# Kernel tuning notes

Measured on AMD Instinct MI355X. Metric: run time of the kernel, lower is better.

The kernel has to match this reference:

```python
import jax, jax.numpy as jnp
import numpy as np

B = 16; L_IN = 512; D_MODEL = 512; N_HEAD = 8; D_K = 128; D_V = 128
D_FF = 2048; N_LAYER = 4; WINDOW = (4, 4, 4); INNER = 5; COV = 4; NUM_SEQ = 128
N_LVL = len(WINDOW) + 1


def _build_mask_sizes():
    # Pyraformer get_mask: intra-scale band + inter-scale parent/child links.
    all_size = [L_IN]
    for w in WINDOW:
        all_size.append(all_size[-1] // w)
    L = sum(all_size)
    vis = np.zeros((L, L), dtype=bool)
    iw = INNER // 2
    starts = [0]
    for s in all_size:
        starts.append(starts[-1] + s)
    for li, sz in enumerate(all_size):
        s = starts[li]
        for i in range(s, s + sz):
            vis[i, max(i - iw, s):min(i + iw + 1, s + sz)] = True
    for li in range(1, len(all_size)):
        s = starts[li]
        for i in range(s, s + all_size[li]):
            l = (s - all_size[li - 1]) + (i - s) * WINDOW[li - 1]
            if i == s + all_size[li] - 1:
                r = s
            else:
                r = (s - all_size[li - 1]) + (i - s + 1) * WINDOW[li - 1]
            vis[i, l:r] = True
            vis[l:r, i] = True
    return ~vis, all_size  # True = blocked


def _build_indexes(all_size):
    # Pyraformer refer_points: for each fine position, its ancestor at each scale.
    idx = np.zeros((L_IN, len(all_size)), dtype=np.int64)
    for i in range(L_IN):
        idx[i, 0] = i
        former = i
        for j in range(1, len(all_size)):
            start = sum(all_size[:j])
            inner = former - (start - all_size[j - 1])
            former = start + min(inner // WINDOW[j - 1], all_size[j] - 1)
            idx[i, j] = former
    return idx


def _layer_norm(x, g, b, eps=1e-5):
    m = x.mean(-1, keepdims=True)
    v = x.var(-1, keepdims=True)
    return (x - m) / jnp.sqrt(v + eps) * g + b


def _conv1d(x, w, stride):  # x: [B,C,L], w: [O,I,K]
    return jax.lax.conv_general_dilated(x, w, (stride,), 'VALID',
                                        dimension_numbers=('NCH', 'OIH', 'NCH'))


def _forward(x, cov_w, cov_b, data_conv_w, down_w, down_b, conv_w, conv_b, bn_g, bn_b,
             up_w, up_b, bln_g, bln_b, wq, wk, wv, fc_w, ln1_g, ln1_b,
             ffn_w1, ffn_b1, ffn_w2, ffn_b2, ln2_g, ln2_b, attn_mask, gather_idx):
    Bsz = x.shape[0]
    # SingleStepEmbedding
    covs = jnp.concatenate([x[:, :, 1:1 + COV], (x[:, :, -1] / NUM_SEQ - 0.5)[..., None]], -1)
    cov_emb = covs @ cov_w + cov_b
    data = x[:, :, 0][:, None, :]                      # [B,1,L]
    data = jnp.concatenate([data[:, :, -1:], data, data[:, :, :1]], -1)  # circular pad k=3
    data_emb = _conv1d(data, data_conv_w, 1).transpose(0, 2, 1)          # [B,L,D]
    i = jnp.arange(D_MODEL)
    vec = jnp.power(10000.0, 2.0 * (i // 2) / D_MODEL)
    ang = jnp.arange(L_IN)[:, None] / vec
    pos_emb = jnp.where(i % 2 == 0, jnp.sin(ang), jnp.cos(ang))
    seq = cov_emb + data_emb + pos_emb[None]
    # Bottleneck_Construct (down -> strided convs -> up -> concat -> LN)
    tmp = (seq @ down_w + down_b).transpose(0, 2, 1)   # [B,d_k,L]
    outs = []
    for s in range(len(WINDOW)):
        tmp = _conv1d(tmp, conv_w[s], WINDOW[s]) + conv_b[s][None, :, None]
        mu = tmp.mean((0, 2), keepdims=True)
        var = tmp.var((0, 2), keepdims=True)
        tmp = (tmp - mu) / jnp.sqrt(var + 1e-5) * bn_g[s][None, :, None] + bn_b[s][None, :, None]
        tmp = jax.nn.elu(tmp)
        outs.append(tmp)
    pyr = jnp.concatenate(outs, axis=2).transpose(0, 2, 1) @ up_w + up_b
    enc = _layer_norm(jnp.concatenate([seq, pyr], axis=1), bln_g, bln_b)  # [B,Ltot,D]
    Lt = enc.shape[1]
    scale = np.float32(1.0 / np.sqrt(D_K))
    for l in range(N_LAYER):
        q = (enc @ wq[l]).reshape(Bsz, Lt, N_HEAD, D_K).transpose(0, 2, 1, 3)
        k = (enc @ wk[l]).reshape(Bsz, Lt, N_HEAD, D_K).transpose(0, 2, 1, 3)
        v = (enc @ wv[l]).reshape(Bsz, Lt, N_HEAD, D_V).transpose(0, 2, 1, 3)
        scores = jnp.einsum('bhqd,bhkd->bhqk', q, k) * scale
        scores = jnp.where(attn_mask[None, None], -1e9, scores)
        attn = jax.nn.softmax(scores, -1)
        o = jnp.einsum('bhqk,bhkd->bhqd', attn, v).transpose(0, 2, 1, 3).reshape(Bsz, Lt, N_HEAD * D_V)
        enc = _layer_norm(o @ fc_w[l] + enc, ln1_g[l], ln1_b[l])  # post-norm
        h = jax.nn.gelu(enc @ ffn_w1[l] + ffn_b1[l], approximate=False) @ ffn_w2[l] + ffn_b2[l]
        enc = _layer_norm(enc + h, ln2_g[l], ln2_b[l])
    # refer_points gather: [B, L_IN, N_LVL*D]
    out = enc[:, gather_idx.reshape(-1), :].reshape(Bsz, L_IN, N_LVL * D_MODEL)
    return out


def setup_inputs() -> dict:
    key = jax.random.key(0)
    ks = iter(jax.random.split(key, 64))

    def nrm(shape, scale=0.02):
        return (jax.random.normal(next(ks), shape) * scale).astype(jnp.float32)

    covs = jax.random.normal(next(ks), (B, L_IN, COV + 1), jnp.float32)
    ids = jax.random.randint(next(ks), (B, L_IN), 0, NUM_SEQ).astype(jnp.float32)
    x = jnp.concatenate([covs, ids[..., None]], -1)  # col0=data, 1..COV=covs, last=series id
    mask_np, all_size = _build_mask_sizes()
    idx = _build_indexes(all_size)
    nw = len(WINDOW)
    return dict(
        x=x,
        cov_w=nrm((COV + 1, D_MODEL)), cov_b=jnp.zeros((D_MODEL,), jnp.float32),
        data_conv_w=nrm((D_MODEL, 1, 3)),
        down_w=nrm((D_MODEL, D_K)), down_b=jnp.zeros((D_K,), jnp.float32),
        conv_w=nrm((nw, D_K, D_K, WINDOW[0])), conv_b=jnp.zeros((nw, D_K), jnp.float32),
        bn_g=jnp.ones((nw, D_K), jnp.float32), bn_b=jnp.zeros((nw, D_K), jnp.float32),
        up_w=nrm((D_K, D_MODEL)), up_b=jnp.zeros((D_MODEL,), jnp.float32),
        bln_g=jnp.ones((D_MODEL,), jnp.float32), bln_b=jnp.zeros((D_MODEL,), jnp.float32),
        wq=nrm((N_LAYER, D_MODEL, N_HEAD * D_K)), wk=nrm((N_LAYER, D_MODEL, N_HEAD * D_K)),
        wv=nrm((N_LAYER, D_MODEL, N_HEAD * D_V)), fc_w=nrm((N_LAYER, N_HEAD * D_V, D_MODEL)),
        ln1_g=jnp.ones((N_LAYER, D_MODEL), jnp.float32), ln1_b=jnp.zeros((N_LAYER, D_MODEL), jnp.float32),
        ffn_w1=nrm((N_LAYER, D_MODEL, D_FF)), ffn_b1=jnp.zeros((N_LAYER, D_FF), jnp.float32),
        ffn_w2=nrm((N_LAYER, D_FF, D_MODEL)), ffn_b2=jnp.zeros((N_LAYER, D_MODEL), jnp.float32),
        ln2_g=jnp.ones((N_LAYER, D_MODEL), jnp.float32), ln2_b=jnp.zeros((N_LAYER, D_MODEL), jnp.float32),
        attn_mask=jnp.asarray(mask_np),
        gather_idx=jnp.asarray(idx),
    )


def reference(x, cov_w, cov_b, data_conv_w, down_w, down_b, conv_w, conv_b, bn_g, bn_b,
              up_w, up_b, bln_g, bln_b, wq, wk, wv, fc_w, ln1_g, ln1_b,
              ffn_w1, ffn_b1, ffn_w2, ffn_b2, ln2_g, ln2_b, attn_mask, gather_idx):
    return _forward(x, cov_w, cov_b, data_conv_w, down_w, down_b, conv_w, conv_b, bn_g, bn_b,
                    up_w, up_b, bln_g, bln_b, wq, wk, wv, fc_w, ln1_g, ln1_b,
                    ffn_w1, ffn_b1, ffn_w2, ffn_b2, ln2_g, ln2_b, attn_mask, gather_idx)
```

## Files before the change

kernel.cpp:

```cpp
#include <hip/hip_runtime.h>
#include <math.h>

typedef unsigned short u16;
typedef unsigned int u32;
typedef __attribute__((ext_vector_type(8))) short s16x8;
typedef __attribute__((ext_vector_type(4))) float f32x4;
typedef __attribute__((ext_vector_type(4))) u32 u32x4;
typedef __attribute__((ext_vector_type(2))) u32 u32x2;

#define LT 680

static __device__ __forceinline__ float bf2f(u16 u) {
  u32 v = ((u32)u) << 16;
  return __builtin_bit_cast(float, v);
}
static __device__ __forceinline__ u16 f2bf(float f) {
  u32 u = __builtin_bit_cast(u32, f);
  u32 r = (u + 0x7FFFu + ((u >> 16) & 1u)) >> 16;
  return (u16)r;
}
static __device__ __forceinline__ float lo16(u32 u) {
  return __builtin_bit_cast(float, u << 16);
}
static __device__ __forceinline__ float hi16(u32 u) {
  return __builtin_bit_cast(float, u & 0xFFFF0000u);
}

static __device__ __forceinline__ void gload16(const u16* g, u16* l) {
  __builtin_amdgcn_global_load_lds(
      (const __attribute__((address_space(1))) u32*)g,
      (__attribute__((address_space(3))) u32*)l, 16, 0, 0);
}

__global__ void detect_k(const u32* __restrict__ blng, int* __restrict__ flag) {
  if (threadIdx.x == 0 && blockIdx.x == 0)
    *flag = (blng[0] == 0x3F803F80u) ? 1 : 0;
}

struct CvtArgs {
  const void* src[20];
  float* dst[20];
  int pre[21];
};

__global__ __launch_bounds__(256) void cvtall_k(CvtArgs a, const int* __restrict__ flag) {
  int i = blockIdx.x * 256 + threadIdx.x;
  if (i >= a.pre[20]) return;
  int s = 0;
#pragma unroll
  for (int k = 1; k <= 20; ++k)
    if (i >= a.pre[k]) s = k;
  int j = i - a.pre[s];
  bool isb = (*flag != 0);
  a.dst[s][j] = isb ? bf2f(((const u16*)a.src[s])[j]) : ((const float*)a.src[s])[j];
}

__global__ __launch_bounds__(256) void tc2_k(const void* __restrict__ S,
                                             u16* __restrict__ D, int K, int N,
                                             size_t sstride, size_t dstride,
                                             const int* __restrict__ flag) {
  __shared__ u16 t[32][33];
  size_t soff = (size_t)blockIdx.z * sstride;
  D += (size_t)blockIdx.z * dstride;
  int nb = blockIdx.x * 32, kb = blockIdx.y * 32;
  int lx = threadIdx.x & 31, ly = threadIdx.x >> 5;
  bool isb = (*flag != 0);
#pragma unroll
  for (int i = 0; i < 4; ++i) {
    size_t idx = soff + (size_t)(kb + ly + 8 * i) * N + nb + lx;
    t[ly + 8 * i][lx] = isb ? ((const u16*)S)[idx] : f2bf(((const float*)S)[idx]);
  }
  __syncthreads();
#pragma unroll
  for (int i = 0; i < 4; ++i)
    D[(size_t)(nb + ly + 8 * i) * K + kb + lx] = t[lx][ly + 8 * i];
}

static __device__ __forceinline__ void reduce2_256(float& a, float& b, float* sm) {
#pragma unroll
  for (int o = 32; o; o >>= 1) { a += __shfl_xor(a, o); b += __shfl_xor(b, o); }
  int w = threadIdx.x >> 6, ln = threadIdx.x & 63;
  if (ln == 0) { sm[w] = a; sm[4 + w] = b; }
  __syncthreads();
  a = sm[0] + sm[1] + sm[2] + sm[3];
  b = sm[4] + sm[5] + sm[6] + sm[7];
  __syncthreads();
}

__global__ __launch_bounds__(256) void emb_k(
    const float* __restrict__ x, const float* __restrict__ covw,
    const float* __restrict__ covb, const float* __restrict__ dw,
    float* __restrict__ seq) {
  int r = blockIdx.x;
  int b = r >> 9, l = r & 511;
  int base = r * 6;
  float c0 = x[base + 1], c1 = x[base + 2];
  float c2 = x[base + 3], c3 = x[base + 4];
  float c4 = x[base + 5] * 0.0078125f - 0.5f;
  int lm = (l + 511) & 511, lp = (l + 1) & 511;
  float dm = x[((b << 9) + lm) * 6];
  float d0 = x[base];
  float dp = x[((b << 9) + lp) * 6];
  for (int d = threadIdx.x; d < 512; d += 256) {
    float cov = c0 * covw[d] + c1 * covw[512 + d] +
                c2 * covw[1024 + d] + c3 * covw[1536 + d] +
                c4 * covw[2048 + d] + covb[d];
    float cv = dm * dw[d * 3] + d0 * dw[d * 3 + 1] + dp * dw[d * 3 + 2];
    float ex = (float)(2 * (d >> 1)) * (1.0f / 512.0f);
    float vec = powf(10000.0f, ex);
    float ang = (float)l / vec;
    float pos = (d & 1) ? cosf(ang) : sinf(ang);
    seq[((size_t)r << 9) + d] = cov + cv + pos;
  }
}

__global__ void tconv_k(const float* __restrict__ w, float* __restrict__ wt) {
  int e = blockIdx.x * 256 + threadIdx.x;
  if (e >= 3 * 512 * 128) return;
  int o = e & 127, ik = (e >> 7) & 511, s = e >> 16;
  wt[e] = w[s * 65536 + o * 512 + ik];
}

__global__ __launch_bounds__(256) void gemm_k(
    const float* __restrict__ A, const float* __restrict__ Bw,
    const float* __restrict__ bias, float* __restrict__ C,
    int M, int N, int K, int act) {
  __shared__ float As[16][64];
  __shared__ float Bs[16][64];
  int tid = threadIdx.x;
  int m0 = blockIdx.y * 64, n0 = blockIdx.x * 64;
  int tx = tid & 15, ty = tid >> 4;
  int la_r = tid >> 2, la_c = (tid & 3) << 2;
  int lb_r = tid >> 4, lb_c = (tid & 15) << 2;
  float acc[4][4] = {};
  for (int k0 = 0; k0 < K; k0 += 16) {
    float4 av = *reinterpret_cast<const float4*>(A + (size_t)(m0 + la_r) * K + k0 + la_c);
    As[la_c + 0][la_r] = av.x;
    As[la_c + 1][la_r] = av.y;
    As[la_c + 2][la_r] = av.z;
    As[la_c + 3][la_r] = av.w;
    float4 bv = *reinterpret_cast<const float4*>(Bw + (size_t)(k0 + lb_r) * N + n0 + lb_c);
    Bs[lb_r][lb_c + 0] = bv.x;
    Bs[lb_r][lb_c + 1] = bv.y;
    Bs[lb_r][lb_c + 2] = bv.z;
    Bs[lb_r][lb_c + 3] = bv.w;
    __syncthreads();
#pragma unroll
    for (int kk = 0; kk < 16; ++kk) {
      float4 a4 = *reinterpret_cast<const float4*>(&As[kk][ty << 2]);
      float4 b4 = *reinterpret_cast<const float4*>(&Bs[kk][tx << 2]);
      float ar[4] = {a4.x, a4.y, a4.z, a4.w};
      float br[4] = {b4.x, b4.y, b4.z, b4.w};
#pragma unroll
      for (int i = 0; i < 4; ++i)
#pragma unroll
        for (int j = 0; j < 4; ++j) acc[i][j] = fmaf(ar[i], br[j], acc[i][j]);
    }
    __syncthreads();
  }
  float bj[4] = {0.f, 0.f, 0.f, 0.f};
  if (bias) {
#pragma unroll
    for (int j = 0; j < 4; ++j) bj[j] = bias[n0 + (tx << 2) + j];
  }
#pragma unroll
  for (int i = 0; i < 4; ++i) {
    float4 o;
    float* op = reinterpret_cast<float*>(&o);
#pragma unroll
    for (int j = 0; j < 4; ++j) op[j] = acc[i][j] + bj[j];
    *reinterpret_cast<float4*>(C + (size_t)(m0 + (ty << 2) + i) * N + n0 + (tx << 2)) = o;
  }
}

static __device__ __forceinline__ f32x4 mfma16(s16x8 a, s16x8 b, f32x4 c) {
  return __builtin_amdgcn_mfma_f32_16x16x32_bf16(a, b, c, 0, 0, 0);
}

__global__ __launch_bounds__(256) void mgemm_k(
    const u16* __restrict__ A, const u16* __restrict__ BT,
    const float* __restrict__ bias, void* __restrict__ C,
    int M, int N, int K, int flags) {
  __shared__ char smem[49152];
  float* st = (float*)smem;
  int tid = threadIdx.x;

  int nN = N >> 7;
  int nwg = gridDim.x;
  int bid = blockIdx.x;
  int qq = nwg >> 3, rr = nwg & 7;
  int xcd = bid & 7, lin = bid >> 3;
  int s_ = (xcd < rr ? xcd * (qq + 1) : rr * (qq + 1) + (xcd - rr) * qq) + lin;
  int m0 = (s_ / nN) << 7, n0 = (s_ % nN) << 7;

  int l = tid & 63, wid = tid >> 6;
  int wr = wid >> 1, wc = wid & 1;
  f32x4 acc[4][4];
#pragma unroll
  for (int i = 0; i < 4; ++i)
#pragma unroll
    for (int j = 0; j < 4; ++j)
#pragma unroll
      for (int r = 0; r < 4; ++r) acc[i][j][r] = 0.f;

  int L8 = l >> 3;
  int p0_ = (l & 7) ^ L8;
  int rloc = 2 * L8 + (p0_ >> 2);
  int cel = (p0_ & 3) << 3;
  const u16* Ag0 = A + (size_t)m0 * K;
  const u16* Bg0 = BT + (size_t)n0 * K;

  auto STAGE = [&](int c, int kt) {
    u16* Ad = (u16*)smem + c * 8192;
    u16* Bd = Ad + 4096;
#pragma unroll
    for (int i = 0; i < 2; ++i) {
      int rg = wid * 32 + i * 16 + rloc;
      gload16(Ag0 + (size_t)rg * K + kt + cel, &Ad[(wid * 16 + i * 8) * 64]);
      gload16(Bg0 + (size_t)rg * K + kt + cel, &Bd[(wid * 16 + i * 8) * 64]);
    }
  };

  int sfrag = (((l & 1) << 2) + (l >> 4)) ^ (((l & 15) >> 1));
  int lhalf = (l & 15) >> 1;

  int nt = K >> 5;
  STAGE(0, 0);
  STAGE(1, 32);
  for (int t = 0; t < nt; ++t) {
    int cur = t % 3;
    if (t + 2 < nt) {
      STAGE((t + 2) % 3, (t + 2) << 5);
      asm volatile("s_waitcnt vmcnt(8)" ::: "memory");
    } else if (t + 1 < nt) {
      asm volatile("s_waitcnt vmcnt(4)" ::: "memory");
    } else {
      asm volatile("s_waitcnt vmcnt(0)" ::: "memory");
    }
    __builtin_amdgcn_s_barrier();
    const u16* Asb = (const u16*)smem + cur * 8192;
    const u16* Bsb = Asb + 4096;
    s16x8 af[4];
#pragma unroll
    for (int fr = 0; fr < 4; ++fr)
      af[fr] = *reinterpret_cast<const s16x8*>(
          &Asb[(wr * 32 + fr * 8 + lhalf) * 64 + sfrag * 8]);
#pragma unroll
    for (int fc = 0; fc < 4; ++fc) {
      s16x8 bf = *reinterpret_cast<const s16x8*>(
          &Bsb[(wc * 32 + fc * 8 + lhalf) * 64 + sfrag * 8]);
#pragma unroll
      for (int fr = 0; fr < 4; ++fr)
        acc[fr][fc] = mfma16(af[fr], bf, acc[fr][fc]);
    }
    asm volatile("s_waitcnt lgkmcnt(0)" ::: "memory");
    __builtin_amdgcn_s_barrier();
  }

  int cl = l & 15, rg2 = l >> 4;
  float bj[4];
#pragma unroll
  for (int fc = 0; fc < 4; ++fc)
    bj[fc] = bias ? bias[n0 + wc * 64 + fc * 16 + cl] : 0.f;
  int sr2 = tid >> 3;
  int scg = (tid & 7) << 4;
  int growb = m0 + ((sr2 >> 4) << 6) + (sr2 & 15);
#pragma unroll
  for (int fr = 0; fr < 4; ++fr) {
#pragma unroll
    for (int fc = 0; fc < 4; ++fc) {
      int col = wc * 64 + fc * 16 + cl;
#pragma unroll
      for (int r = 0; r < 4; ++r) {
        float v = acc[fr][fc][r] + bj[fc];
        if (flags & 2) {
          float zz = 1.5957691f * fmaf(0.044715f * v, v * v, v);
          v = v / (1.0f + __expf(-zz));
        }
        st[(wr * 16 + rg2 * 4 + r) * 132 + col] = v;
      }
    }
    __syncthreads();
    int gr = growb + fr * 16;
    if (flags & 1) {
      u32x4 o0, o1;
      u16* p0 = (u16*)&o0; u16* p1 = (u16*)&o1;
#pragma unroll
      for (int i = 0; i < 8; ++i) p0[i] = f2bf(st[sr2 * 132 + scg + i]);
#pragma unroll
      for (int i = 0; i < 8; ++i) p1[i] = f2bf(st[sr2 * 132 + scg + 8 + i]);
      u16* dst = (u16*)C + (size_t)gr * N + n0 + scg;
      __builtin_nontemporal_store(o0, reinterpret_cast<u32x4*>(dst));
      __builtin_nontemporal_store(o1, reinterpret_cast<u32x4*>(dst + 8));
    } else {
      float* dst = (float*)C + (size_t)gr * N + n0 + scg;
#pragma unroll
      for (int i = 0; i < 4; ++i)
        __builtin_nontemporal_store(
            *reinterpret_cast<const f32x4*>(&st[sr2 * 132 + scg + 4 * i]),
            reinterpret_cast<f32x4*>(dst + 4 * i));
    }
    __syncthreads();
  }
}

__global__ __launch_bounds__(256) void mg64_k(
    const u16* __restrict__ A, const u16* __restrict__ BT,
    const float* __restrict__ bias, float* __restrict__ C,
    int M, int N, int K) {
  __shared__ char smem[49152];
  float* st = (float*)smem;
  int tid = threadIdx.x;

  int nN = N >> 6;
  int nwg = gridDim.x;
  int bid = blockIdx.x;
  int qq = nwg >> 3, rr = nwg & 7;
  int xcd = bid & 7, lin = bid >> 3;
  int s_ = (xcd < rr ? xcd * (qq + 1) : rr * (qq + 1) + (xcd - rr) * qq) + lin;
  int m0 = (s_ / nN) << 6, n0 = (s_ % nN) << 6;

  int l = tid & 63, wid = tid >> 6;
  f32x4 acc[4];
#pragma unroll
  for (int j = 0; j < 4; ++j)
#pragma unroll
    for (int r = 0; r < 4; ++r) acc[j][r] = 0.f;

  int row8 = l >> 3, cp = l & 7;
  int cg = (cp ^ (row8 & 7)) << 3;
  const u16* Ag0 = A + (size_t)m0 * K;
  const u16* Bg0 = BT + (size_t)n0 * K;

  auto STAGE = [&](int c, int kt) {
    u16* Ad = (u16*)smem + c * 8192;
    u16* Bd = Ad + 4096;
#pragma unroll
    for (int i = 0; i < 2; ++i) {
      int r = wid * 16 + i * 8 + row8;
      gload16(Ag0 + (size_t)r * K + kt + cg, &Ad[(wid * 16 + i * 8) * 64]);
      gload16(Bg0 + (size_t)r * K + kt + cg, &Bd[(wid * 16 + i * 8) * 64]);
    }
  };

  int nt = K >> 6;
  STAGE(0, 0);
  STAGE(1, 64);
  for (int t = 0; t < nt; ++t) {
    int cur = t % 3;
    if (t + 2 < nt) {
      STAGE((t + 2) % 3, (t + 2) << 6);
      asm volatile("s_waitcnt vmcnt(8)" ::: "memory");
    } else if (t + 1 < nt) {
      asm volatile("s_waitcnt vmcnt(4)" ::: "memory");
    } else {
      asm volatile("s_waitcnt vmcnt(0)" ::: "memory");
    }
    __builtin_amdgcn_s_barrier();
    const u16* Asb = (const u16*)smem + cur * 8192;
    const u16* Bsb = Asb + 4096;
#pragma unroll
    for (int kk = 0; kk < 2; ++kk) {
      int kc = ((kk * 4 + (l >> 4)) ^ (l & 7)) * 8;
      s16x8 af = *reinterpret_cast<const s16x8*>(
          &Asb[(wid * 16 + (l & 15)) * 64 + kc]);
#pragma unroll
      for (int fc = 0; fc < 4; ++fc) {
        s16x8 bf = *reinterpret_cast<const s16x8*>(
            &Bsb[(fc * 16 + (l & 15)) * 64 + kc]);
        acc[fc] = mfma16(af, bf, acc[fc]);
      }
    }
    asm volatile("s_waitcnt lgkmcnt(0)" ::: "memory");
    __builtin_amdgcn_s_barrier();
  }

  int cl = l & 15, rg = l >> 4;
  float bj[4];
#pragma unroll
  for (int fc = 0; fc < 4; ++fc)
    bj[fc] = bias ? bias[n0 + fc * 16 + cl] : 0.f;
#pragma unroll
  for (int fc = 0; fc < 4; ++fc)
#pragma unroll
    for (int r = 0; r < 4; ++r)
      st[(wid * 16 + rg * 4 + r) * 80 + fc * 16 + cl] = acc[fc][r] + bj[fc];
  __syncthreads();
  int lr = tid >> 2;
  int lq = (tid & 3) << 2;
  float* dst = C + (size_t)(m0 + lr) * N + n0;
#pragma unroll
  for (int i = 0; i < 4; ++i)
    __builtin_nontemporal_store(
        *reinterpret_cast<const f32x4*>(&st[lr * 80 + lq + 16 * i]),
        reinterpret_cast<f32x4*>(dst + lq + 16 * i));
}

__global__ void im2col_k(const float* __restrict__ Y, float* __restrict__ X,
                         int Ti, int To) {
  int e = blockIdx.x * 256 + threadIdx.x;
  int ik = e & 511;
  int bt = e >> 9;
  int b = bt / To, t = bt - b * To;
  int i = ik >> 2, k = ik & 3;
  X[e] = Y[((size_t)(b * Ti + (t << 2) + k) << 7) + i];
}

__global__ __launch_bounds__(256) void bnelu_k(float* __restrict__ Y,
                                               const float* __restrict__ g,
                                               const float* __restrict__ be, int Ms) {
  __shared__ float sm[8];
  int ch = blockIdx.x;
  float s = 0.f, s2 = 0.f;
  for (int i = threadIdx.x; i < Ms; i += 256) {
    float v = Y[((size_t)i << 7) + ch];
    s += v; s2 += v * v;
  }
  reduce2_256(s, s2, sm);
  float mu = s / (float)Ms;
  float var = s2 / (float)Ms - mu * mu;
  float inv = rsqrtf(var + 1e-5f);
  float ga = g[ch], bb = be[ch];
  for (int i = threadIdx.x; i < Ms; i += 256) {
    float v = (Y[((size_t)i << 7) + ch] - mu) * inv * ga + bb;
    Y[((size_t)i << 7) + ch] = (v > 0.f) ? v : (expf(v) - 1.0f);
  }
}

__global__ void scat_k(const float* __restrict__ Y, float* __restrict__ cat,
                       int Ts, int off) {
  int e = blockIdx.x * 256 + threadIdx.x;
  int i = e & 127;
  int bt = e >> 7;
  int b = bt / Ts, t = bt - b * Ts;
  cat[((size_t)(b * 168 + off + t) << 7) + i] = Y[e];
}

__global__ __launch_bounds__(256) void catln_k(
    const float* __restrict__ seq, const float* __restrict__ pyr,
    const float* __restrict__ g, const float* __restrict__ be,
    float* __restrict__ out, u16* __restrict__ outb) {
  __shared__ float sm[8];
  int row = blockIdx.x;
  int b = row / LT, j = row - b * LT;
  const float* src = (j < 512) ? (seq + ((size_t)(b * 512 + j) << 9))
                               : (pyr + ((size_t)(b * 168 + j - 512) << 9));
  int t = threadIdx.x;
  float x0 = src[t], x1 = src[t + 256];
  float s = x0 + x1, s2 = x0 * x0 + x1 * x1;
  reduce2_256(s, s2, sm);
  float mu = s * 0.001953125f;
  float var = s2 * 0.001953125f - mu * mu;
  float inv = rsqrtf(var + 1e-5f);
  size_t ob = (size_t)row << 9;
  float v0 = (x0 - mu) * inv * g[t] + be[t];
  float v1 = (x1 - mu) * inv * g[t + 256] + be[t + 256];
  out[ob + t] = v0; out[ob + t + 256] = v1;
  outb[ob + t] = f2bf(v0); outb[ob + t + 256] = f2bf(v1);
}

__global__ __launch_bounds__(256) void lnres_k(
    const float* __restrict__ A, const float* __restrict__ R,
    const float* __restrict__ g, const float* __restrict__ be,
    float* __restrict__ O, u16* __restrict__ Ob) {
  __shared__ float sm[8];
  int row = blockIdx.x;
  size_t base = (size_t)row << 9;
  int t = threadIdx.x;
  float x0 = A[base + t] + R[base + t];
  float x1 = A[base + t + 256] + R[base + t + 256];
  float s = x0 + x1, s2 = x0 * x0 + x1 * x1;
  reduce2_256(s, s2, sm);
  float mu = s * 0.001953125f;
  float var = s2 * 0.001953125f - mu * mu;
  float inv = rsqrtf(var + 1e-5f);
  float v0 = (x0 - mu) * inv * g[t] + be[t];
  float v1 = (x1 - mu) * inv * g[t + 256] + be[t + 256];
  O[base + t] = v0; O[base + t + 256] = v1;
  Ob[base + t] = f2bf(v0); Ob[base + t + 256] = f2bf(v1);
}

__global__ __launch_bounds__(256) void attn_k(const u16* __restrict__ QKV,
                                              u16* __restrict__ O) {
  int cpx = gridDim.x >> 3;
  int bq = (blockIdx.x & 7) * cpx + (blockIdx.x >> 3);
  int b = bq / LT, q = bq - b * LT;
  int lane = threadIdx.x & 63, wv = threadIdx.x >> 6;
  int half = lane >> 5, t4 = (lane & 31) << 2;
  int h = (wv << 1) + half;
  int lvl = (q < 512) ? 0 : (q < 640) ? 1 : (q < 672) ? 2 : 3;
  int Sl = (lvl == 0) ? 0 : (lvl == 1) ? 512 : (lvl == 2) ? 640 : 672;
  int SZl = (lvl == 0) ? 512 : (lvl == 1) ? 128 : (lvl == 2) ? 32 : 8;
  int p = q - Sl;
  int Sc = (lvl == 1) ? 0 : (lvl == 2) ? 512 : 640;
  int Sp = (lvl == 0) ? 512 : (lvl == 1) ? 640 : 672;
  int tg[10];
  bool vd[10];
#pragma unroll
  for (int jj = 0; jj < 10; ++jj) {
    int tgt; bool valid;
    if (jj < 5) { int pp = p - 2 + jj; valid = (pp >= 0 && pp < SZl); tgt = Sl + pp; }
    else if (jj < 9) { valid = (lvl > 0); tgt = Sc + p * 4 + (jj - 5); }
    else { valid = (lvl < 3); tgt = Sp + (p >> 2); }
    if (!valid) tgt = q;
    tg[jj] = tgt; vd[jj] = valid;
  }
  size_t hoff = h * 128 + t4;
  u32x2 qv = *reinterpret_cast<const u32x2*>(QKV + (size_t)bq * 3072 + hoff);
  float q0 = lo16(qv.x), q1 = hi16(qv.x), q2 = lo16(qv.y), q3 = hi16(qv.y);
  size_t base3 = (size_t)b * LT;
  float sc[10];
  float mx = -1e30f;
#pragma unroll
  for (int jj = 0; jj < 10; ++jj) {
    u32x2 kv = *reinterpret_cast<const u32x2*>(
        QKV + (base3 + tg[jj]) * 3072 + 1024 + hoff);
    float pr = q0 * lo16(kv.x) + q1 * hi16(kv.x) + q2 * lo16(kv.y) + q3 * hi16(kv.y);
#pragma unroll
    for (int o = 16; o; o >>= 1) pr += __shfl_xor(pr, o);
    float sv = vd[jj] ? pr * 0.08838834764831845f : -1e30f;
    sc[jj] = sv;
    mx = fmaxf(mx, sv);
  }
  float den = 0.f;
#pragma unroll
  for (int jj = 0; jj < 10; ++jj) { sc[jj] = expf(sc[jj] - mx); den += sc[jj]; }
  float invd = 1.0f / den;
  float o0 = 0.f, o1 = 0.f, o2 = 0.f, o3 = 0.f;
#pragma unroll
  for (int jj = 0; jj < 10; ++jj) {
    u32x2 vv = *reinterpret_cast<const u32x2*>(
        QKV + (base3 + tg[jj]) * 3072 + 2048 + hoff);
    float w = sc[jj] * invd;
    o0 = fmaf(w, lo16(vv.x), o0);
    o1 = fmaf(w, hi16(vv.x), o1);
    o2 = fmaf(w, lo16(vv.y), o2);
    o3 = fmaf(w, hi16(vv.y), o3);
  }
  u32x2 ov;
  ov.x = (u32)f2bf(o0) | ((u32)f2bf(o1) << 16);
  ov.y = (u32)f2bf(o2) | ((u32)f2bf(o3) << 16);
  *reinterpret_cast<u32x2*>(O + (size_t)bq * 1024 + hoff) = ov;
}

__global__ void gather_k(const float* __restrict__ enc, void* __restrict__ out,
                         const int* __restrict__ flag) {
  int e = blockIdx.x * 256 + threadIdx.x;
  int d = e & 511;
  int lvl = (e >> 9) & 3;
  int i = (e >> 11) & 511;
  int b = e >> 20;
  int g = (lvl == 0) ? i
        : (lvl == 1) ? (512 + (i >> 2))
        : (lvl == 2) ? (640 + (i >> 4))
                     : (672 + (i >> 6));
  float v = enc[(((size_t)b * LT + g) << 9) + d];
  if (*flag) ((u16*)out)[e] = f2bf(v);
  else       ((float*)out)[e] = v;
}

extern "C" void kernel_launch(void* const* d_in, const int* in_sizes, int n_in,
                              void* d_out, int out_size, void* d_ws, size_t ws_size,
                              hipStream_t stream) {
  float* ws = (float*)d_ws;
  size_t off = 0;
  auto alloc = [&](size_t n) { float* p = ws + off; off += (n + 63) & ~(size_t)63; return p; };

  int* flag = (int*)alloc(64);

  static const int cvt_n[26] = {
      49152, 2560, 512, 1536, 65536, 128, 196608, 384, 384, 384,
      65536, 512, 512, 512, 2097152, 2097152, 2097152, 2097152, 2048, 2048,
      4194304, 8192, 4194304, 2048, 2048, 2048};
  float* cf[26];
  for (int i = 0; i < 26; ++i) {
    if (i == 14 || i == 15 || i == 16 || i == 17 || i == 20 || i == 22) {
      cf[i] = nullptr;
      continue;
    }
    cf[i] = alloc(cvt_n[i]);
  }

  float* cwt     = alloc(196608);
  float* enc     = alloc((size_t)10880 * 512);
  float* tmp     = alloc((size_t)10880 * 512);
  u16*   encb    = (u16*)alloc((size_t)10880 * 512 / 2);
  u16*   qkv     = (u16*)alloc((size_t)10880 * 3072 / 2);
  u16*   attnout = (u16*)alloc((size_t)10880 * 1024 / 2);
  u16*   qkvw    = (u16*)alloc((size_t)4 * 3072 * 512 / 2);
  u16*   fcT     = (u16*)alloc((size_t)4 * 512 * 1024 / 2);
  u16*   w1T     = (u16*)alloc((size_t)4 * 2048 * 512 / 2);
  u16*   w2T     = (u16*)alloc((size_t)4 * 512 * 2048 / 2);
  u16*   H1      = qkv;

  float* seq   = (float*)qkv;
  float* pyr   = seq + 4194304;
  float* tdown = pyr + 1376256;
  float* xcol  = tdown + 1048576;
  float* ya    = xcol + 1048576;
  float* yb    = ya + 262144;
  float* yc    = yb + 65536;
  float* cat   = yc + 16384;

  detect_k<<<1, 64, 0, stream>>>((const u32*)d_in[12], flag);
  {
    static const int segs[20] = {0,1,2,3,4,5,6,7,8,9,10,11,12,13,18,19,21,23,24,25};
    CvtArgs a;
    int acc_ = 0;
    for (int k = 0; k < 20; ++k) {
      int i = segs[k];
      a.src[k] = d_in[i];
      a.dst[k] = cf[i];
      a.pre[k] = acc_;
      acc_ += cvt_n[i];
    }
    a.pre[20] = acc_;
    cvtall_k<<<(acc_ + 255) / 256, 256, 0, stream>>>(a, flag);
  }

  const float *x = cf[0], *covw = cf[1], *covb = cf[2], *dconvw = cf[3],
              *downw = cf[4], *downb = cf[5], *convw = cf[6], *convb = cf[7],
              *bng = cf[8], *bnb = cf[9], *upw = cf[10], *upb = cf[11],
              *blng = cf[12], *blnb = cf[13], *ln1g = cf[18], *ln1b = cf[19],
              *b1 = cf[21], *b2 = cf[23], *ln2g = cf[24], *ln2b = cf[25];

  tc2_k<<<dim3(32, 16, 4), 256, 0, stream>>>(d_in[14], qkvw,           512, 1024, 524288, 1572864, flag);
  tc2_k<<<dim3(32, 16, 4), 256, 0, stream>>>(d_in[15], qkvw + 524288,  512, 1024, 524288, 1572864, flag);
  tc2_k<<<dim3(32, 16, 4), 256, 0, stream>>>(d_in[16], qkvw + 1048576, 512, 1024, 524288, 1572864, flag);
  tc2_k<<<dim3(16, 32, 4), 256, 0, stream>>>(d_in[17], fcT,  1024, 512, 524288, 524288, flag);
  tc2_k<<<dim3(64, 16, 4), 256, 0, stream>>>(d_in[20], w1T,  512, 2048, 1048576, 1048576, flag);
  tc2_k<<<dim3(16, 64, 4), 256, 0, stream>>>(d_in[22], w2T,  2048, 512, 1048576, 1048576, flag);

  emb_k<<<8192, 256, 0, stream>>>(x, covw, covb, dconvw, seq);
  tconv_k<<<(3 * 512 * 128 + 255) / 256, 256, 0, stream>>>(convw, cwt);

  gemm_k<<<dim3(2, 128), 256, 0, stream>>>(seq, downw, downb, tdown, 8192, 128, 512, 0);
  im2col_k<<<(16 * 128 * 512) / 256, 256, 0, stream>>>(tdown, xcol, 512, 128);
  gemm_k<<<dim3(2, 32), 256, 0, stream>>>(xcol, cwt, convb, ya, 2048, 128, 512, 0);
  bnelu_k<<<128, 256, 0, stream>>>(ya, bng, bnb, 2048);
  scat_k<<<(2048 * 128) / 256, 256, 0, stream>>>(ya, cat, 128, 0);
  im2col_k<<<(16 * 32 * 512) / 256, 256, 0, stream>>>(ya, xcol, 128, 32);
  gemm_k<<<dim3(2, 8), 256, 0, stream>>>(xcol, cwt + 65536, convb + 128, yb, 512, 128, 512, 0);
  bnelu_k<<<128, 256, 0, stream>>>(yb, bng + 128, bnb + 128, 512);
  scat_k<<<(512 * 128) / 256, 256, 0, stream>>>(yb, cat, 32, 128);
  im2col_k<<<(16 * 8 * 512) / 256, 256, 0, stream>>>(yb, xcol, 32, 8);
  gemm_k<<<dim3(2, 2), 256, 0, stream>>>(xcol, cwt + 131072, convb + 256, yc, 128, 128, 512, 0);
  bnelu_k<<<128, 256, 0, stream>>>(yc, bng + 256, bnb + 256, 128);
  scat_k<<<(128 * 128) / 256, 256, 0, stream>>>(yc, cat, 8, 160);
  gemm_k<<<dim3(8, 42), 256, 0, stream>>>(cat, upw, upb, pyr, 2688, 512, 128, 0);
  catln_k<<<10880, 256, 0, stream>>>(seq, pyr, blng, blnb, enc, encb);

  for (int l = 0; l < 4; ++l) {
    const u16* qw  = qkvw + (size_t)l * 3072 * 512;
    const u16* fw  = fcT + (size_t)l * 524288;
    const u16* w1w = w1T + (size_t)l * 1048576;
    const u16* w2w = w2T + (size_t)l * 1048576;
    mgemm_k<<<85 * 24, 256, 0, stream>>>(encb, qw, nullptr, qkv, 10880, 3072, 512, 1);
    attn_k<<<16 * LT, 256, 0, stream>>>(qkv, attnout);
    mg64_k<<<170 * 8, 256, 0, stream>>>(attnout, fw, nullptr, tmp, 10880, 512, 1024);
    lnres_k<<<10880, 256, 0, stream>>>(tmp, enc, ln1g + l * 512, ln1b + l * 512, enc, encb);
    mgemm_k<<<85 * 16, 256, 0, stream>>>(encb, w1w, b1 + l * 2048, H1, 10880, 2048, 512, 3);
    mg64_k<<<170 * 8, 256, 0, stream>>>(H1, w2w, b2 + l * 512, tmp, 10880, 512, 2048);
    lnres_k<<<10880, 256, 0, stream>>>(tmp, enc, ln2g + l * 512, ln2b + l * 512, enc, encb);
  }

  gather_k<<<(16 * 512 * 2048) / 256, 256, 0, stream>>>(enc, d_out, flag);
}
```

Before: 1.230 ms.

## Move bottleneck-conv GEMMs to bf16 MFMA and store FFN/FC outputs in bf16

Replaces the scalar fp32 tiled GEMM used for down-projection, the three strided convolutions and the up-projection with the existing bf16 MFMA GEMM kernel. The weights are pre-transposed or converted to bf16, and im2col, the scatter and the embedding now also emit bf16 copies. The positional encoding table is computed once in a separate kernel instead of per element inside the embedding. The mg64 output used before layernorm is stored as bf16 to halve its write and read traffic, at some cost in precision.

Result: faster. 1.129 ms (-8.2%).

```diff
diff --git a/kernel.cpp b/kernel.cpp
--- a/kernel.cpp
+++ b/kernel.cpp
@@ -76,6 +76,13 @@
     D[(size_t)(nb + ly + 8 * i) * K + kb + lx] = t[lx][ly + 8 * i];
 }
 
+__global__ void cvb_k(const void* __restrict__ S, u16* __restrict__ D, int n,
+                      const int* __restrict__ flag) {
+  int i = blockIdx.x * 256 + threadIdx.x;
+  if (i >= n) return;
+  D[i] = (*flag) ? ((const u16*)S)[i] : f2bf(((const float*)S)[i]);
+}
+
 static __device__ __forceinline__ void reduce2_256(float& a, float& b, float* sm) {
 #pragma unroll
   for (int o = 32; o; o >>= 1) { a += __shfl_xor(a, o); b += __shfl_xor(b, o); }
@@ -87,10 +94,21 @@
   __syncthreads();
 }
 
+__global__ __launch_bounds__(256) void pos_k(float* __restrict__ post) {
+  int l = blockIdx.x;
+  int d0 = threadIdx.x << 1;
+  float ex = (float)d0 * (1.0f / 512.0f);
+  float vec = powf(10000.0f, ex);
+  float ang = (float)l / vec;
+  post[(l << 9) + d0] = sinf(ang);
+  post[(l << 9) + d0 + 1] = cosf(ang);
+}
+
 __global__ __launch_bounds__(256) void emb_k(
     const float* __restrict__ x, const float* __restrict__ covw,
     const float* __restrict__ covb, const float* __restrict__ dw,
-    float* __restrict__ seq) {
+    const float* __restrict__ post, float* __restrict__ seq,
+    u16* __restrict__ seqb) {
   int r = blockIdx.x;
   int b = r >> 9, l = r & 511;
   int base = r * 6;
@@ -106,70 +124,9 @@
                 c2 * covw[1024 + d] + c3 * covw[1536 + d] +
                 c4 * covw[2048 + d] + covb[d];
     float cv = dm * dw[d * 3] + d0 * dw[d * 3 + 1] + dp * dw[d * 3 + 2];
-    float ex = (float)(2 * (d >> 1)) * (1.0f / 512.0f);
-    float vec = powf(10000.0f, ex);
-    float ang = (float)l / vec;
-    float pos = (d & 1) ? cosf(ang) : sinf(ang);
-    seq[((size_t)r << 9) + d] = cov + cv + pos;
-  }
-}
-
-__global__ void tconv_k(const float* __restrict__ w, float* __restrict__ wt) {
-  int e = blockIdx.x * 256 + threadIdx.x;
-  if (e >= 3 * 512 * 128) return;
-  int o = e & 127, ik = (e >> 7) & 511, s = e >> 16;
-  wt[e] = w[s * 65536 + o * 512 + ik];
-}
-
-__global__ __launch_bounds__(256) void gemm_k(
-    const float* __restrict__ A, const float* __restrict__ Bw,
-    const float* __restrict__ bias, float* __restrict__ C,
-    int M, int N, int K, int act) {
-  __shared__ float As[16][64];
-  __shared__ float Bs[16][64];
-  int tid = threadIdx.x;
-  int m0 = blockIdx.y * 64, n0 = blockIdx.x * 64;
-  int tx = tid & 15, ty = tid >> 4;
-  int la_r = tid >> 2, la_c = (tid & 3) << 2;
-  int lb_r = tid >> 4, lb_c = (tid & 15) << 2;
-  float acc[4][4] = {};
-  for (int k0 = 0; k0 < K; k0 += 16) {
-    float4 av = *reinterpret_cast<const float4*>(A + (size_t)(m0 + la_r) * K + k0 + la_c);
-    As[la_c + 0][la_r] = av.x;
-    As[la_c + 1][la_r] = av.y;
-    As[la_c + 2][la_r] = av.z;
-    As[la_c + 3][la_r] = av.w;
-    float4 bv = *reinterpret_cast<const float4*>(Bw + (size_t)(k0 + lb_r) * N + n0 + lb_c);
-    Bs[lb_r][lb_c + 0] = bv.x;
-    Bs[lb_r][lb_c + 1] = bv.y;
-    Bs[lb_r][lb_c + 2] = bv.z;
-    Bs[lb_r][lb_c + 3] = bv.w;
-    __syncthreads();
-#pragma unroll
-    for (int kk = 0; kk < 16; ++kk) {
-      float4 a4 = *reinterpret_cast<const float4*>(&As[kk][ty << 2]);
-      float4 b4 = *reinterpret_cast<const float4*>(&Bs[kk][tx << 2]);
-      float ar[4] = {a4.x, a4.y, a4.z, a4.w};
-      float br[4] = {b4.x, b4.y, b4.z, b4.w};
-#pragma unroll
-      for (int i = 0; i < 4; ++i)
-#pragma unroll
-        for (int j = 0; j < 4; ++j) acc[i][j] = fmaf(ar[i], br[j], acc[i][j]);
-    }
-    __syncthreads();
-  }
-  float bj[4] = {0.f, 0.f, 0.f, 0.f};
-  if (bias) {
-#pragma unroll
-    for (int j = 0; j < 4; ++j) bj[j] = bias[n0 + (tx << 2) + j];
-  }
-#pragma unroll
-  for (int i = 0; i < 4; ++i) {
-    float4 o;
-    float* op = reinterpret_cast<float*>(&o);
-#pragma unroll
-    for (int j = 0; j < 4; ++j) op[j] = acc[i][j] + bj[j];
-    *reinterpret_cast<float4*>(C + (size_t)(m0 + (ty << 2) + i) * N + n0 + (tx << 2)) = o;
+    float v = cov + cv + post[(l << 9) + d];
+    seq[((size_t)r << 9) + d] = v;
+    seqb[((size_t)r << 9) + d] = f2bf(v);
   }
 }
 
@@ -306,7 +263,7 @@
 
 __global__ __launch_bounds__(256) void mg64_k(
     const u16* __restrict__ A, const u16* __restrict__ BT,
-    const float* __restrict__ bias, float* __restrict__ C,
+    const float* __restrict__ bias, u16* __restrict__ C,
     int M, int N, int K) {
   __shared__ char smem[49152];
   float* st = (float*)smem;
@@ -386,24 +343,28 @@
     for (int r = 0; r < 4; ++r)
       st[(wid * 16 + rg * 4 + r) * 80 + fc * 16 + cl] = acc[fc][r] + bj[fc];
   __syncthreads();
-  int lr = tid >> 2;
-  int lq = (tid & 3) << 2;
-  float* dst = C + (size_t)(m0 + lr) * N + n0;
-#pragma unroll
-  for (int i = 0; i < 4; ++i)
+  int rr2 = tid >> 3;
+  int cc2 = (tid & 7) << 3;
+#pragma unroll
+  for (int ps = 0; ps < 2; ++ps) {
+    int row = rr2 + ps * 32;
+    u32x4 o;
+    u16* pp = (u16*)&o;
+#pragma unroll
+    for (int i = 0; i < 8; ++i) pp[i] = f2bf(st[row * 80 + cc2 + i]);
     __builtin_nontemporal_store(
-        *reinterpret_cast<const f32x4*>(&st[lr * 80 + lq + 16 * i]),
-        reinterpret_cast<f32x4*>(dst + lq + 16 * i));
-}
-
-__global__ void im2col_k(const float* __restrict__ Y, float* __restrict__ X,
-                         int Ti, int To) {
+        o, reinterpret_cast<u32x4*>(C + (size_t)(m0 + row) * N + n0 + cc2));
+  }
+}
+
+__global__ void im2colb_k(const float* __restrict__ Y, u16* __restrict__ X,
+                          int Ti, int To) {
   int e = blockIdx.x * 256 + threadIdx.x;
   int ik = e & 511;
   int bt = e >> 9;
   int b = bt / To, t = bt - b * To;
   int i = ik >> 2, k = ik & 3;
-  X[e] = Y[((size_t)(b * Ti + (t << 2) + k) << 7) + i];
+  X[e] = f2bf(Y[((size_t)(b * Ti + (t << 2) + k) << 7) + i]);
 }
 
 __global__ __launch_bounds__(256) void bnelu_k(float* __restrict__ Y,
@@ -428,12 +389,15 @@
 }
 
 __global__ void scat_k(const float* __restrict__ Y, float* __restrict__ cat,
-                       int Ts, int off) {
+                       u16* __restrict__ catb, int Ts, int off) {
   int e = blockIdx.x * 256 + threadIdx.x;
   int i = e & 127;
   int bt = e >> 7;
   int b = bt / Ts, t = bt - b * Ts;
-  cat[((size_t)(b * 168 + off + t) << 7) + i] = Y[e];
+  float v = Y[e];
+  size_t idx = ((size_t)(b * 168 + off + t) << 7) + i;
+  cat[idx] = v;
+  catb[idx] = f2bf(v);
 }
 
 __global__ __launch_bounds__(256) void catln_k(
@@ -460,15 +424,15 @@
 }
 
 __global__ __launch_bounds__(256) void lnres_k(
-    const float* __restrict__ A, const float* __restrict__ R,
+    const u16* __restrict__ A, const float* __restrict__ R,
     const float* __restrict__ g, const float* __restrict__ be,
     float* __restrict__ O, u16* __restrict__ Ob) {
   __shared__ float sm[8];
   int row = blockIdx.x;
   size_t base = (size_t)row << 9;
   int t = threadIdx.x;
-  float x0 = A[base + t] + R[base + t];
-  float x1 = A[base + t + 256] + R[base + t + 256];
+  float x0 = bf2f(A[base + t]) + R[base + t];
+  float x1 = bf2f(A[base + t + 256]) + R[base + t + 256];
   float s = x0 + x1, s2 = x0 * x0 + x1 * x1;
   reduce2_256(s, s2, sm);
   float mu = s * 0.001953125f;
@@ -574,16 +538,17 @@
       4194304, 8192, 4194304, 2048, 2048, 2048};
   float* cf[26];
   for (int i = 0; i < 26; ++i) {
-    if (i == 14 || i == 15 || i == 16 || i == 17 || i == 20 || i == 22) {
+    if (i == 4 || i == 6 || i == 10 || i == 14 || i == 15 || i == 16 ||
+        i == 17 || i == 20 || i == 22) {
       cf[i] = nullptr;
       continue;
     }
     cf[i] = alloc(cvt_n[i]);
   }
 
-  float* cwt     = alloc(196608);
+  float* post    = alloc((size_t)512 * 512);
   float* enc     = alloc((size_t)10880 * 512);
-  float* tmp     = alloc((size_t)10880 * 512);
+  u16*   tmp     = (u16*)alloc((size_t)10880 * 512 / 2);
   u16*   encb    = (u16*)alloc((size_t)10880 * 512 / 2);
   u16*   qkv     = (u16*)alloc((size_t)10880 * 3072 / 2);
   u16*   attnout = (u16*)alloc((size_t)10880 * 1024 / 2);
@@ -591,36 +556,44 @@
   u16*   fcT     = (u16*)alloc((size_t)4 * 512 * 1024 / 2);
   u16*   w1T     = (u16*)alloc((size_t)4 * 2048 * 512 / 2);
   u16*   w2T     = (u16*)alloc((size_t)4 * 512 * 2048 / 2);
+  u16*   dwT     = (u16*)alloc((size_t)128 * 512 / 2);
+  u16*   upT     = (u16*)alloc((size_t)512 * 128 / 2);
+  u16*   cwb     = (u16*)alloc((size_t)3 * 128 * 512 / 2);
   u16*   H1      = qkv;
 
   float* seq   = (float*)qkv;
   float* pyr   = seq + 4194304;
   float* tdown = pyr + 1376256;
-  float* xcol  = tdown + 1048576;
-  float* ya    = xcol + 1048576;
+  float* ya    = tdown + 1048576;
   float* yb    = ya + 262144;
   float* yc    = yb + 65536;
   float* cat   = yc + 16384;
+  u16*   seqb  = (u16*)(cat + 344064);
+  u16*   xcolb = seqb + 4194304;
+  u16*   catb  = xcolb + 1048576;
 
   detect_k<<<1, 64, 0, stream>>>((const u32*)d_in[12], flag);
   {
-    static const int segs[20] = {0,1,2,3,4,5,6,7,8,9,10,11,12,13,18,19,21,23,24,25};
+    static const int segs[17] = {0,1,2,3,5,7,8,9,11,12,13,18,19,21,23,24,25};
     CvtArgs a;
     int acc_ = 0;
-    for (int k = 0; k < 20; ++k) {
+    for (int k = 0; k < 17; ++k) {
       int i = segs[k];
       a.src[k] = d_in[i];
       a.dst[k] = cf[i];
       a.pre[k] = acc_;
       acc_ += cvt_n[i];
     }
-    a.pre[20] = acc_;
+    for (int k = 17; k <= 20; ++k) {
+      a.pre[k] = acc_;
+      if (k < 20) { a.src[k] = d_in[0]; a.dst[k] = cf[0]; }
+    }
     cvtall_k<<<(acc_ + 255) / 256, 256, 0, stream>>>(a, flag);
   }
 
   const float *x = cf[0], *covw = cf[1], *covb = cf[2], *dconvw = cf[3],
-              *downw = cf[4], *downb = cf[5], *convw = cf[6], *convb = cf[7],
-              *bng = cf[8], *bnb = cf[9], *upw = cf[10], *upb = cf[11],
+              *downb = cf[5], *convb = cf[7],
+              *bng = cf[8], *bnb = cf[9], *upb = cf[11],
               *blng = cf[12], *blnb = cf[13], *ln1g = cf[18], *ln1b = cf[19],
               *b1 = cf[21], *b2 = cf[23], *ln2g = cf[24], *ln2b = cf[25];
 
@@ -630,24 +603,27 @@
   tc2_k<<<dim3(16, 32, 4), 256, 0, stream>>>(d_in[17], fcT,  1024, 512, 524288, 524288, flag);
   tc2_k<<<dim3(64, 16, 4), 256, 0, stream>>>(d_in[20], w1T,  512, 2048, 1048576, 1048576, flag);
   tc2_k<<<dim3(16, 64, 4), 256, 0, stream>>>(d_in[22], w2T,  2048, 512, 1048576, 1048576, flag);
-
-  emb_k<<<8192, 256, 0, stream>>>(x, covw, covb, dconvw, seq);
-  tconv_k<<<(3 * 512 * 128 + 255) / 256, 256, 0, stream>>>(convw, cwt);
-
-  gemm_k<<<dim3(2, 128), 256, 0, stream>>>(seq, downw, downb, tdown, 8192, 128, 512, 0);
-  im2col_k<<<(16 * 128 * 512) / 256, 256, 0, stream>>>(tdown, xcol, 512, 128);
-  gemm_k<<<dim3(2, 32), 256, 0, stream>>>(xcol, cwt, convb, ya, 2048, 128, 512, 0);
+  tc2_k<<<dim3(4, 16, 1), 256, 0, stream>>>(d_in[4],  dwT, 512, 128, 0, 0, flag);
+  tc2_k<<<dim3(16, 4, 1), 256, 0, stream>>>(d_in[10], upT, 128, 512, 0, 0, flag);
+  cvb_k<<<(196608 + 255) / 256, 256, 0, stream>>>(d_in[6], cwb, 196608, flag);
+
+  pos_k<<<512, 256, 0, stream>>>(post);
+  emb_k<<<8192, 256, 0, stream>>>(x, covw, covb, dconvw, post, seq, seqb);
+
+  mgemm_k<<<64, 256, 0, stream>>>(seqb, dwT, downb, tdown, 8192, 128, 512, 0);
+  im2colb_k<<<(16 * 128 * 512) / 256, 256, 0, stream>>>(tdown, xcolb, 512, 128);
+  mgemm_k<<<16, 256, 0, stream>>>(xcolb, cwb, convb, ya, 2048, 128, 512, 0);
   bnelu_k<<<128, 256, 0, stream>>>(ya, bng, bnb, 2048);
-  scat_k<<<(2048 * 128) / 256, 256, 0, stream>>>(ya, cat, 128, 0);
-  im2col_k<<<(16 * 32 * 512) / 256, 256, 0, stream>>>(ya, xcol, 128, 32);
-  gemm_k<<<dim3(2, 8), 256, 0, stream>>>(xcol, cwt + 65536, convb + 128, yb, 512, 128, 512, 0);
+  scat_k<<<(2048 * 128) / 256, 256, 0, stream>>>(ya, cat, catb, 128, 0);
+  im2colb_k<<<(16 * 32 * 512) / 256, 256, 0, stream>>>(ya, xcolb, 128, 32);
+  mgemm_k<<<4, 256, 0, stream>>>(xcolb, cwb + 65536, convb + 128, yb, 512, 128, 512, 0);
   bnelu_k<<<128, 256, 0, stream>>>(yb, bng + 128, bnb + 128, 512);
-  scat_k<<<(512 * 128) / 256, 256, 0, stream>>>(yb, cat, 32, 128);
-  im2col_k<<<(16 * 8 * 512) / 256, 256, 0, stream>>>(yb, xcol, 32, 8);
-  gemm_k<<<dim3(2, 2), 256, 0, stream>>>(xcol, cwt + 131072, convb + 256, yc, 128, 128, 512, 0);
+  scat_k<<<(512 * 128) / 256, 256, 0, stream>>>(yb, cat, catb, 32, 128);
+  im2colb_k<<<(16 * 8 * 512) / 256, 256, 0, stream>>>(yb, xcolb, 32, 8);
+  mgemm_k<<<1, 256, 0, stream>>>(xcolb, cwb + 131072, convb + 256, yc, 128, 128, 512, 0);
   bnelu_k<<<128, 256, 0, stream>>>(yc, bng + 256, bnb + 256, 128);
-  scat_k<<<(128 * 128) / 256, 256, 0, stream>>>(yc, cat, 8, 160);
-  gemm_k<<<dim3(8, 42), 256, 0, stream>>>(cat, upw, upb, pyr, 2688, 512, 128, 0);
+  scat_k<<<(128 * 128) / 256, 256, 0, stream>>>(yc, cat, catb, 8, 160);
+  mgemm_k<<<21 * 4, 256, 0, stream>>>(catb, upT, upb, pyr, 2688, 512, 128, 0);
   catln_k<<<10880, 256, 0, stream>>>(seq, pyr, blng, blnb, enc, encb);
 
   for (int l = 0; l < 4; ++l) {
```
